# Kernel tuning notes

Hardware: AMD Instinct MI355X
Metric: run time of the kernel (lower is better)

The kernel has to match this reference:

```python
import jax, jax.numpy as jnp
import numpy as np

DATA_SIZE = 32
WIDTH = 128
DEPTH = 4
BATCH = 4096
IN_DIM = 1                      # input_prev_data=False -> 1
OUT_DIM = 2 * DATA_SIZE         # predict_uncertainty=True
DIMS = [IN_DIM] + [WIDTH] * DEPTH + [OUT_DIM]
TOTAL_PARAMS = sum(DIMS[i + 1] * DIMS[i] + DIMS[i + 1] for i in range(len(DIMS) - 1))  # 58048


def setup_inputs() -> dict:
    key = jax.random.key(0)
    k1, k2 = jax.random.split(key)
    x = jax.random.normal(k1, (BATCH, IN_DIM), dtype=jnp.float32)
    flat_weights = jax.random.normal(k2, (BATCH, TOTAL_PARAMS), dtype=jnp.float32) * 0.1
    return {"x": x, "flat_weights": flat_weights}


def reference(x, flat_weights):
    # Per-sample MLP: each batch element carries its own flattened weights,
    # sliced in nn.Module named_parameters order: (i.weight, i.bias) per Linear.
    y = x
    idx = 0
    n_layers = len(DIMS) - 1
    B = flat_weights.shape[0]
    for i in range(n_layers):
        d_in, d_out = DIMS[i], DIMS[i + 1]
        W = flat_weights[:, idx:idx + d_out * d_in].reshape(B, d_out, d_in)
        idx += d_out * d_in
        b = flat_weights[:, idx:idx + d_out]
        idx += d_out
        y = jnp.einsum('bi,boi->bo', y, W) + b   # batched GEMV
        if i < n_layers - 1:
            y = jax.nn.silu(y)                   # 'swish' hidden activation
    # predict_uncertainty head: chunk -> tanh mean, clamp/exp std, concat
    mean, logvar = jnp.split(y, 2, axis=-1)
    mean = jnp.tanh(mean)                         # final_activation 'tanh'
    std = jnp.exp(0.5 * jnp.clip(logvar, -4.0, 4.0))
    return jnp.concatenate([mean, std], axis=-1)
```

## Files before the change

kernel.cpp:

```cpp
#include <hip/hip_runtime.h>
#include <math.h>


#define WIDTH 128
#define OUTD  64
#define TOTAL_PARAMS 58048

__device__ __forceinline__ float silu(float a) {
    return a / (1.0f + expf(-a));
}

__global__ __launch_bounds__(256)
void rootmlp_kernel(const float* __restrict__ x,
                    const float* __restrict__ w,
                    float* __restrict__ out) {
    const int b = blockIdx.x;
    const int t = threadIdx.x;
    const int l = t & 7;
    const int g = t >> 3;
    const float* __restrict__ wb = w + (size_t)b * TOTAL_PARAMS;

    __shared__ __align__(16) float ybuf[2][WIDTH];

    if (t < WIDTH) {
        float a = wb[t] * x[b] + wb[WIDTH + t];
        ybuf[0][t] = silu(a);
    }
    __syncthreads();

    int idx = 2 * WIDTH;
    int cur = 0;

    #pragma unroll 1
    for (int layer = 0; layer < 3; ++layer) {
        const float* __restrict__ W    = wb + idx;
        const float* __restrict__ bias = W + WIDTH * WIDTH;
        const float* __restrict__ ycur = ybuf[cur];

        #pragma unroll
        for (int p = 0; p < 4; ++p) {
            const int j = p * 32 + g;
            const float4* __restrict__ Wrow = (const float4*)(W + j * WIDTH);
            float a = 0.0f;
            #pragma unroll
            for (int i = 0; i < 4; ++i) {
                const float4 wv = Wrow[l + i * 8];
                const float4 yv = *(const float4*)(ycur + l * 4 + i * 32);
                a += wv.x * yv.x + wv.y * yv.y + wv.z * yv.z + wv.w * yv.w;
            }
            a += __shfl_xor(a, 1);
            a += __shfl_xor(a, 2);
            a += __shfl_xor(a, 4);
            if (l == 0) {
                ybuf[cur ^ 1][j] = silu(a + bias[j]);
            }
        }
        __syncthreads();
        cur ^= 1;
        idx += WIDTH * WIDTH + WIDTH;
    }

    {
        const float* __restrict__ W    = wb + idx;
        const float* __restrict__ bias = W + OUTD * WIDTH;
        const float* __restrict__ ycur = ybuf[cur];

        #pragma unroll
        for (int p = 0; p < 2; ++p) {
            const int j = p * 32 + g;
            const float4* __restrict__ Wrow = (const float4*)(W + j * WIDTH);
            float a = 0.0f;
            #pragma unroll
            for (int i = 0; i < 4; ++i) {
                const float4 wv = Wrow[l + i * 8];
                const float4 yv = *(const float4*)(ycur + l * 4 + i * 32);
                a += wv.x * yv.x + wv.y * yv.y + wv.z * yv.z + wv.w * yv.w;
            }
            a += __shfl_xor(a, 1);
            a += __shfl_xor(a, 2);
            a += __shfl_xor(a, 4);
            if (l == 0) {
                a += bias[j];
                float r;
                if (j < 32) {
                    r = tanhf(a);
                } else {
                    float lv = fminf(fmaxf(a, -4.0f), 4.0f);
                    r = expf(0.5f * lv);
                }
                out[(size_t)b * OUTD + j] = r;
            }
        }
    }
}

extern "C" void kernel_launch(void* const* d_in, const int* in_sizes, int n_in,
                              void* d_out, int out_size, void* d_ws, size_t ws_size,
                              hipStream_t stream) {
    const float* x = (const float*)d_in[0];
    const float* w = (const float*)d_in[1];
    float* out = (float*)d_out;

    const int batch = in_sizes[0];
    rootmlp_kernel<<<batch, 256, 0, stream>>>(x, w, out);
}
```

Measured before the change: 166.1 us.

## Map one wavefront per sample and replace block barriers with LDS waitcnt

Each sample is now handled by a single 64-lane wavefront instead of a 256-thread block, with four samples per block and a private LDS buffer per wave. Block-wide __syncthreads is replaced by an s_waitcnt lgkmcnt(0) fence, on the assumption that a wavefront executes in lockstep so its own LDS writes are visible once the wait completes. Each wave now loops over 16 output groups per layer instead of 4. This gives more in-flight loads per wave and removes barrier stalls, but the workload is memory-bound on streaming weights, so any gain depends on latency hiding. The final head is staged through LDS so all 64 lanes apply the activation and write the output coalesced.

```diff
diff --git a/kernel.cpp b/kernel.cpp
--- a/kernel.cpp
+++ b/kernel.cpp
@@ -10,23 +10,32 @@
     return a / (1.0f + expf(-a));
 }
 
-__global__ __launch_bounds__(256)
+__device__ __forceinline__ void lds_fence() {
+    asm volatile("s_waitcnt lgkmcnt(0)" ::: "memory");
+}
+
+__global__ __launch_bounds__(256, 4)
 void rootmlp_kernel(const float* __restrict__ x,
                     const float* __restrict__ w,
                     float* __restrict__ out) {
-    const int b = blockIdx.x;
-    const int t = threadIdx.x;
-    const int l = t & 7;
-    const int g = t >> 3;
+    const int wv   = threadIdx.x >> 6;
+    const int lane = threadIdx.x & 63;
+    const int b    = blockIdx.x * 4 + wv;
+    const int l    = lane & 7;
+    const int g    = lane >> 3;
     const float* __restrict__ wb = w + (size_t)b * TOTAL_PARAMS;
 
-    __shared__ __align__(16) float ybuf[2][WIDTH];
+    __shared__ __align__(16) float ybuf[4][2][WIDTH];
+    float (*yb)[WIDTH] = ybuf[wv];
 
-    if (t < WIDTH) {
-        float a = wb[t] * x[b] + wb[WIDTH + t];
-        ybuf[0][t] = silu(a);
+    {
+        const float xv = x[b];
+        float a0 = wb[lane]      * xv + wb[128 + lane];
+        float a1 = wb[64 + lane] * xv + wb[192 + lane];
+        yb[0][lane]      = silu(a0);
+        yb[0][64 + lane] = silu(a1);
     }
-    __syncthreads();
+    lds_fence();
 
     int idx = 2 * WIDTH;
     int cur = 0;
@@ -35,27 +44,28 @@
     for (int layer = 0; layer < 3; ++layer) {
         const float* __restrict__ W    = wb + idx;
         const float* __restrict__ bias = W + WIDTH * WIDTH;
-        const float* __restrict__ ycur = ybuf[cur];
+        const float* ycur = yb[cur];
+        float*       ynxt = yb[cur ^ 1];
 
         #pragma unroll
-        for (int p = 0; p < 4; ++p) {
-            const int j = p * 32 + g;
+        for (int p = 0; p < 16; ++p) {
+            const int j = p * 8 + g;
             const float4* __restrict__ Wrow = (const float4*)(W + j * WIDTH);
             float a = 0.0f;
             #pragma unroll
             for (int i = 0; i < 4; ++i) {
-                const float4 wv = Wrow[l + i * 8];
-                const float4 yv = *(const float4*)(ycur + l * 4 + i * 32);
-                a += wv.x * yv.x + wv.y * yv.y + wv.z * yv.z + wv.w * yv.w;
+                const float4 wvv = Wrow[l + i * 8];
+                const float4 yv  = *(const float4*)(ycur + l * 4 + i * 32);
+                a += wvv.x * yv.x + wvv.y * yv.y + wvv.z * yv.z + wvv.w * yv.w;
             }
             a += __shfl_xor(a, 1);
             a += __shfl_xor(a, 2);
             a += __shfl_xor(a, 4);
             if (l == 0) {
-                ybuf[cur ^ 1][j] = silu(a + bias[j]);
+                ynxt[j] = silu(a + bias[j]);
             }
         }
-        __syncthreads();
+        lds_fence();
         cur ^= 1;
         idx += WIDTH * WIDTH + WIDTH;
     }
@@ -63,34 +73,38 @@
     {
         const float* __restrict__ W    = wb + idx;
         const float* __restrict__ bias = W + OUTD * WIDTH;
-        const float* __restrict__ ycur = ybuf[cur];
+        const float* ycur = yb[cur];
+        float*       ystg = yb[cur ^ 1];
 
         #pragma unroll
-        for (int p = 0; p < 2; ++p) {
-            const int j = p * 32 + g;
+        for (int p = 0; p < 8; ++p) {
+            const int j = p * 8 + g;
             const float4* __restrict__ Wrow = (const float4*)(W + j * WIDTH);
             float a = 0.0f;
             #pragma unroll
             for (int i = 0; i < 4; ++i) {
-                const float4 wv = Wrow[l + i * 8];
-                const float4 yv = *(const float4*)(ycur + l * 4 + i * 32);
-                a += wv.x * yv.x + wv.y * yv.y + wv.z * yv.z + wv.w * yv.w;
+                const float4 wvv = Wrow[l + i * 8];
+                const float4 yv  = *(const float4*)(ycur + l * 4 + i * 32);
+                a += wvv.x * yv.x + wvv.y * yv.y + wvv.z * yv.z + wvv.w * yv.w;
             }
             a += __shfl_xor(a, 1);
             a += __shfl_xor(a, 2);
             a += __shfl_xor(a, 4);
             if (l == 0) {
-                a += bias[j];
-                float r;
-                if (j < 32) {
-                    r = tanhf(a);
-                } else {
-                    float lv = fminf(fmaxf(a, -4.0f), 4.0f);
-                    r = expf(0.5f * lv);
-                }
-                out[(size_t)b * OUTD + j] = r;
+                ystg[j] = a + bias[j];
             }
         }
+        lds_fence();
+
+        float a = ystg[lane];
+        float r;
+        if (lane < 32) {
+            r = tanhf(a);
+        } else {
+            float lv = fminf(fmaxf(a, -4.0f), 4.0f);
+            r = expf(0.5f * lv);
+        }
+        out[(size_t)b * OUTD + lane] = r;
     }
 }
 
@@ -102,5 +116,5 @@
     float* out = (float*)d_out;
 
     const int batch = in_sizes[0];
-    rootmlp_kernel<<<batch, 256, 0, stream>>>(x, w, out);
+    rootmlp_kernel<<<batch / 4, 256, 0, stream>>>(x, w, out);
 }
```

Measured after the change: 163.6 us. About the same (-1.5%).
